# Performance work log

Hardware: AMD Instinct MI355X
Metric: run time of the kernel (lower is better)

## Reference

```python
import jax, jax.numpy as jnp
import numpy as np

B, H, L = 1024, 32, 3
D_S, D_ID = 512, 128
D_STEER = 3 * D_S + D_ID  # 1664
D_HID = 2048
HS, DQ = 16, 64
HDQ = HS * DQ  # 1024


def setup_inputs() -> dict:
    key = jax.random.key(0)
    ks = jax.random.split(key, 18)
    n = lambda k, shape, std: jax.random.normal(k, shape, dtype=jnp.float32) * std
    inp = {
        "x": jax.random.normal(ks[0], (B * H, D_STEER), dtype=jnp.float32),
        "id_in": jax.random.normal(ks[1], (B * H, D_ID), dtype=jnp.float32),
        # per-head content MLP params
        "in_proj_w": n(ks[2], (H, D_STEER, D_S), 0.014),
        "in_proj_b": jnp.zeros((H, D_S), jnp.float32),
        "norm_w": jnp.ones((H, L, D_S), jnp.float32),
        "up_w": n(ks[3], (H, L, D_S, D_HID), 0.014),
        "up_b": jnp.zeros((H, L, D_HID), jnp.float32),
        "down_w": n(ks[4], (H, L, D_HID, D_S), (2.0 / D_HID) ** 0.5),
        "down_b": jnp.zeros((H, L, D_S), jnp.float32),
        # q_proj: Linear(D_steer, 2*HDQ) -> GELU -> Linear(2*HDQ, HDQ)
        "q1_w": n(ks[5], (D_STEER, 2 * HDQ), 0.014),
        "q1_b": jnp.zeros((2 * HDQ,), jnp.float32),
        "q2_w": n(ks[6], (2 * HDQ, HDQ), 0.02),
        "q2_b": jnp.zeros((HDQ,), jnp.float32),
        # k_proj: Linear(D_id, 2*HDQ) -> GELU -> Linear(2*HDQ, HDQ)
        "k1_w": n(ks[7], (D_ID, 2 * HDQ), 0.014),
        "k1_b": jnp.zeros((2 * HDQ,), jnp.float32),
        "k2_w": n(ks[8], (2 * HDQ, HDQ), 0.02),
        "k2_b": jnp.zeros((HDQ,), jnp.float32),
    }
    return inp


def _per_head_mlp(x, in_proj_w, in_proj_b, norm_w, up_w, up_b, down_w, down_b):
    # x: [B*H, D_steer] -> [B*H, D_s]
    bh = x.shape[0]
    b = bh // H
    xh = x.reshape(b, H, D_STEER)
    h = jnp.einsum("bhd,hde->bhe", xh, in_proj_w) + in_proj_b[None]
    for i in range(norm_w.shape[1]):
        rms = jax.lax.rsqrt(jnp.mean(h * h, axis=-1, keepdims=True) + 1e-6)
        xn = h * rms * norm_w[:, i][None]
        hid = jax.nn.gelu(jnp.einsum("bhd,hde->bhe", xn, up_w[:, i]) + up_b[:, i][None], approximate=False)
        h = h + jnp.einsum("bhd,hde->bhe", hid, down_w[:, i]) + down_b[:, i][None]
    return h.reshape(bh, D_S)


def reference(x, id_in, in_proj_w, in_proj_b, norm_w, up_w, up_b, down_w, down_b,
              q1_w, q1_b, q2_w, q2_b, k1_w, k1_b, k2_w, k2_b):
    content = _per_head_mlp(x, in_proj_w, in_proj_b, norm_w, up_w, up_b, down_w, down_b)
    q = jax.nn.gelu(x @ q1_w + q1_b, approximate=False) @ q2_w + q2_b
    k = jax.nn.gelu(id_in @ k1_w + k1_b, approximate=False) @ k2_w + k2_b
    # concat outputs: [B*H, D_s + HDQ + HDQ]
    return jnp.concatenate([content, q, k], axis=-1)
```

## Files before the change

kernel.cpp:

```cpp
#include <hip/hip_runtime.h>
#include <hip/hip_bf16.h>
#include <math.h>

#define HH 32
#define LL 3
#define DS 512
#define DID 128
#define DSTEER 1664
#define DHID 2048
#define HDQ 1024
#define BHROWS 32768

typedef __attribute__((ext_vector_type(8))) short short8;
typedef __attribute__((ext_vector_type(4))) float f32x4;

typedef const __attribute__((address_space(1))) unsigned int* gptr_t;
typedef __attribute__((address_space(3))) unsigned int* lptr_t;

#define BAR() __builtin_amdgcn_s_barrier()
#define SB()  __builtin_amdgcn_sched_barrier(0)
#define VMCNT8() asm volatile("s_waitcnt vmcnt(8)")
#define VMCNT2() asm volatile("s_waitcnt vmcnt(2)")
#define VMCNT0() asm volatile("s_waitcnt vmcnt(0)")

__device__ __forceinline__ unsigned short f2bf(float f) {
  union { float f; unsigned int u; } x; x.f = f;
  unsigned int r = (x.u + 0x7FFFu + ((x.u >> 16) & 1u)) >> 16;
  return (unsigned short)r;
}
__device__ __forceinline__ unsigned int pk2(float a, float b) {
  return (unsigned int)f2bf(a) | ((unsigned int)f2bf(b) << 16);
}
__device__ __forceinline__ float gelu_exact(float v) {
  return 0.5f * v * (1.0f + erff(v * 0.70710678118654752440f));
}

__global__ void cvt_bf16_kernel(const float4* __restrict__ in, uint2* __restrict__ out, long n4) {
  long i = (long)blockIdx.x * blockDim.x + threadIdx.x;
  long stride = (long)gridDim.x * blockDim.x;
  for (; i < n4; i += stride) {
    float4 v = in[i];
    uint2 o; o.x = pk2(v.x, v.y); o.y = pk2(v.z, v.w);
    out[i] = o;
  }
}

__global__ void transpose_cvt_kernel(const float* __restrict__ in, long long in_bstride,
                                     unsigned short* __restrict__ out, long long out_bstride,
                                     int R, int C) {
  __shared__ float t[64][33];
  const int r0 = blockIdx.y * 32;
  const int c0 = blockIdx.x * 64;
  const float* bin = in + (long long)blockIdx.z * in_bstride;
  unsigned short* bout = out + (long long)blockIdx.z * out_bstride;
  const int tid = threadIdx.x;
  const int col = tid & 63, rr = tid >> 6;
  #pragma unroll
  for (int j = 0; j < 8; j++) {
    int r = j * 4 + rr;
    t[col][r] = bin[(size_t)(r0 + r) * C + c0 + col];
  }
  __syncthreads();
  const int rq = (tid & 7) * 4;
  const int cc = tid >> 3;
  #pragma unroll
  for (int j = 0; j < 2; j++) {
    int c = j * 32 + cc;
    float v0 = t[c][rq], v1 = t[c][rq + 1], v2 = t[c][rq + 2], v3 = t[c][rq + 3];
    uint2 o; o.x = pk2(v0, v1); o.y = pk2(v2, v3);
    *(uint2*)&bout[(size_t)(c0 + c) * R + r0 + rq] = o;
  }
}

__global__ void rms_scale_kernel(const float* __restrict__ h,
                                 const float* __restrict__ norm_w,
                                 unsigned short* __restrict__ xn, int layer) {
  int gw = (int)((blockIdx.x * blockDim.x + threadIdx.x) >> 6);
  int lane = threadIdx.x & 63;
  if (gw >= BHROWS) return;
  int head = gw & (HH - 1);
  const float4* hr = (const float4*)(h + (size_t)gw * DS);
  float4 v0 = hr[lane * 2], v1 = hr[lane * 2 + 1];
  float ss = v0.x*v0.x + v0.y*v0.y + v0.z*v0.z + v0.w*v0.w
           + v1.x*v1.x + v1.y*v1.y + v1.z*v1.z + v1.w*v1.w;
  #pragma unroll
  for (int off = 32; off > 0; off >>= 1) ss += __shfl_xor(ss, off, 64);
  float r = rsqrtf(ss * (1.0f / DS) + 1e-6f);
  const float4* nw = (const float4*)(norm_w + ((size_t)head * LL + layer) * DS);
  float4 w0 = nw[lane * 2], w1 = nw[lane * 2 + 1];
  uint4 o;
  o.x = pk2(v0.x * r * w0.x, v0.y * r * w0.y);
  o.y = pk2(v0.z * r * w0.z, v0.w * r * w0.w);
  o.z = pk2(v1.x * r * w1.x, v1.y * r * w1.y);
  o.w = pk2(v1.z * r * w1.z, v1.w * r * w1.w);
  *(uint4*)(xn + (size_t)gw * DS + (size_t)lane * 8) = o;
}

template<int EPI>
__global__ __launch_bounds__(512, 2)
void gemm256_kernel(const unsigned short* __restrict__ A, int lda, int rstep,
                    const unsigned short* __restrict__ Bt, int ldb, long long b_hstride,
                    const float* __restrict__ bias, int bias_hstride,
                    const float* __restrict__ resid, int ldr,
                    void* __restrict__ Cv, int ldc, int K) {
  __shared__ unsigned short lds[2 * 2 * 256 * 64];
  const int tid = threadIdx.x;
  const int lane = tid & 63;
  const int wave = tid >> 6;
  const int wr = wave >> 2, wc = wave & 3;
  const int head = blockIdx.z;
  const int gx = gridDim.x;
  const int nwg = gx * gridDim.y;
  int wgid = blockIdx.y * gx + blockIdx.x;
  { int cpx = nwg >> 3; wgid = (wgid & 7) * cpx + (wgid >> 3); }
  const int tn = wgid % gx, tm = wgid / gx;

  const int l3 = lane >> 3;
  const int gslot = ((lane & 7) ^ l3) * 8;
  const int mbase = wave * 8 + l3;
  const int nbase = (wave >> 2) * 64 + (wave & 3) * 8 + l3;
  const unsigned short* pA = A + ((size_t)(tm * 256 + mbase) * rstep + head) * lda + gslot;
  const unsigned short* pB = Bt + (size_t)head * b_hstride
                               + (size_t)(tn * 256 + nbase) * ldb + gslot;
  const size_t aBlk = (size_t)64 * rstep * lda;

  const int physk0 = ((lane >> 4) ^ (lane & 7)) * 8;
  const int physk1 = ((4 + (lane >> 4)) ^ (lane & 7)) * 8;
  const int aRow = wr * 128 + (lane & 15);
  const int bRow = wc * 32 + (lane & 15);

  auto stageA = [&](unsigned short* dstA, int h, size_t kels) {
    #pragma unroll
    for (int i = 0; i < 2; ++i)
      __builtin_amdgcn_global_load_lds(
          (gptr_t)(pA + (size_t)(i * 2 + h) * aBlk + kels),
          (lptr_t)(dstA + ((i * 2 + h) * 64 + wave * 8) * 64), 16, 0, 0);
  };
  auto stageB = [&](unsigned short* dstB, int h, size_t kels) {
    #pragma unroll
    for (int i = 0; i < 2; ++i)
      __builtin_amdgcn_global_load_lds(
          (gptr_t)(pB + (size_t)(i * 128 + h * 32) * ldb + kels),
          (lptr_t)(dstB + (h * 128 + i * 64 + wave * 8) * 64), 16, 0, 0);
  };

  f32x4 acc[8][4];
  #pragma unroll
  for (int i = 0; i < 8; ++i)
    #pragma unroll
    for (int j = 0; j < 4; ++j) acc[i][j] = (f32x4){0.f, 0.f, 0.f, 0.f};
  short8 a[4][2], b[4][2];

  const int T = K >> 6;
  stageA(lds, 0, 0);
  stageB(lds + 16384, 0, 0);
  stageB(lds + 16384, 1, 0);
  stageA(lds, 1, 0);
  stageA(lds + 32768, 0, 64);
  stageB(lds + 32768 + 16384, 0, 64);
  stageB(lds + 32768 + 16384, 1, 64);
  VMCNT8();
  SB();
  BAR();

  for (int t = 0; t < T; ++t) {
    unsigned short* rA = lds + (t & 1) * 32768;
    unsigned short* rB = rA + 16384;
    unsigned short* nA = lds + ((t + 1) & 1) * 32768;
    const size_t k1 = (size_t)(t + 1) * 64;
    const size_t k2 = (size_t)(t + 2) * 64;
    const bool m1 = (t + 1 < T), m2 = (t + 2 < T);

    #pragma unroll
    for (int j = 0; j < 2; ++j) {
      b[j][0] = *(const short8*)&rB[(bRow + j * 16) * 64 + physk0];
      b[j][1] = *(const short8*)&rB[(bRow + j * 16) * 64 + physk1];
    }
    #pragma unroll
    for (int i = 0; i < 4; ++i) {
      a[i][0] = *(const short8*)&rA[(aRow + i * 16) * 64 + physk0];
      a[i][1] = *(const short8*)&rA[(aRow + i * 16) * 64 + physk1];
    }
    if (m1) stageA(nA, 1, k1);
    __builtin_amdgcn_s_setprio(1);
    #pragma unroll
    for (int i = 0; i < 4; ++i)
      #pragma unroll
      for (int j = 0; j < 2; ++j) {
        acc[i][j] = __builtin_amdgcn_mfma_f32_16x16x32_bf16(a[i][0], b[j][0], acc[i][j], 0, 0, 0);
        acc[i][j] = __builtin_amdgcn_mfma_f32_16x16x32_bf16(a[i][1], b[j][1], acc[i][j], 0, 0, 0);
      }
    __builtin_amdgcn_s_setprio(0);
    BAR();

    #pragma unroll
    for (int j = 0; j < 2; ++j) {
      b[2 + j][0] = *(const short8*)&rB[(128 + bRow + j * 16) * 64 + physk0];
      b[2 + j][1] = *(const short8*)&rB[(128 + bRow + j * 16) * 64 + physk1];
    }
    __builtin_amdgcn_s_setprio(1);
    #pragma unroll
    for (int i = 0; i < 4; ++i)
      #pragma unroll
      for (int j = 0; j < 2; ++j) {
        acc[i][2 + j] = __builtin_amdgcn_mfma_f32_16x16x32_bf16(a[i][0], b[2 + j][0], acc[i][2 + j], 0, 0, 0);
        acc[i][2 + j] = __builtin_amdgcn_mfma_f32_16x16x32_bf16(a[i][1], b[2 + j][1], acc[i][2 + j], 0, 0, 0);
      }
    __builtin_amdgcn_s_setprio(0);
    if (m1) { VMCNT8(); } else { VMCNT0(); }
    SB();
    BAR();

    #pragma unroll
    for (int i = 0; i < 4; ++i) {
      a[i][0] = *(const short8*)&rA[(aRow + (4 + i) * 16) * 64 + physk0];
      a[i][1] = *(const short8*)&rA[(aRow + (4 + i) * 16) * 64 + physk1];
    }
    if (m2) { stageA(rA, 0, k2); stageB(rB, 0, k2); }
    __builtin_amdgcn_s_setprio(1);
    #pragma unroll
    for (int i = 0; i < 4; ++i)
      #pragma unroll
      for (int j = 0; j < 2; ++j) {
        acc[4 + i][2 + j] = __builtin_amdgcn_mfma_f32_16x16x32_bf16(a[i][0], b[2 + j][0], acc[4 + i][2 + j], 0, 0, 0);
        acc[4 + i][2 + j] = __builtin_amdgcn_mfma_f32_16x16x32_bf16(a[i][1], b[2 + j][1], acc[4 + i][2 + j], 0, 0, 0);
      }
    __builtin_amdgcn_s_setprio(0);
    BAR();

    if (m2) stageB(rB, 1, k2);
    __builtin_amdgcn_s_setprio(1);
    #pragma unroll
    for (int i = 0; i < 4; ++i)
      #pragma unroll
      for (int j = 0; j < 2; ++j) {
        acc[4 + i][j] = __builtin_amdgcn_mfma_f32_16x16x32_bf16(a[i][0], b[j][0], acc[4 + i][j], 0, 0, 0);
        acc[4 + i][j] = __builtin_amdgcn_mfma_f32_16x16x32_bf16(a[i][1], b[j][1], acc[4 + i][j], 0, 0, 0);
      }
    __builtin_amdgcn_s_setprio(0);
    if (m2) { VMCNT8(); } else if (m1) { VMCNT2(); }
    SB();
    BAR();
  }

  const float* bptr = bias + (size_t)head * bias_hstride;
  #pragma unroll
  for (int i = 0; i < 8; ++i) {
    #pragma unroll
    for (int j = 0; j < 4; ++j) {
      #pragma unroll
      for (int r = 0; r < 4; ++r) {
        int rowt = wr * 128 + i * 16 + (lane >> 4) * 4 + r;
        int colt = wc * 64 + j * 16 + (lane & 15);
        int col = tn * 256 + colt;
        size_t crow = (size_t)(tm * 256 + rowt) * rstep + head;
        float v = acc[i][j][r] + bptr[col];
        if (EPI == 1) {
          ((unsigned short*)Cv)[crow * (size_t)ldc + col] = f2bf(gelu_exact(v));
        } else if (EPI == 2) {
          v += resid[crow * (size_t)ldr + col];
          ((float*)Cv)[crow * (size_t)ldc + col] = v;
        } else {
          ((float*)Cv)[crow * (size_t)ldc + col] = v;
        }
      }
    }
  }
}

extern "C" void kernel_launch(void* const* d_in, const int* in_sizes, int n_in,
                              void* d_out, int out_size, void* d_ws, size_t ws_size,
                              hipStream_t stream) {
  const float* x         = (const float*)d_in[0];
  const float* id_in     = (const float*)d_in[1];
  const float* in_proj_w = (const float*)d_in[2];
  const float* in_proj_b = (const float*)d_in[3];
  const float* norm_w    = (const float*)d_in[4];
  const float* up_w      = (const float*)d_in[5];
  const float* up_b      = (const float*)d_in[6];
  const float* down_w    = (const float*)d_in[7];
  const float* down_b    = (const float*)d_in[8];
  const float* q1_w      = (const float*)d_in[9];
  const float* q1_b      = (const float*)d_in[10];
  const float* q2_w      = (const float*)d_in[11];
  const float* q2_b      = (const float*)d_in[12];
  const float* k1_w      = (const float*)d_in[13];
  const float* k1_b      = (const float*)d_in[14];
  const float* k2_w      = (const float*)d_in[15];
  const float* k2_b      = (const float*)d_in[16];
  float* out = (float*)d_out;

  char* ws = (char*)d_ws;
  unsigned short* x_bf  = (unsigned short*)ws; ws += (size_t)BHROWS * DSTEER * 2;
  unsigned short* id_bf = (unsigned short*)ws; ws += (size_t)BHROWS * DID * 2;
  float*          hbuf  = (float*)ws;          ws += (size_t)BHROWS * DS * 4;
  unsigned short* xn    = (unsigned short*)ws; ws += (size_t)BHROWS * DS * 2;
  unsigned short* hid   = (unsigned short*)ws; ws += (size_t)BHROWS * DHID * 2;
  unsigned short* wbuf  = (unsigned short*)ws; ws += (size_t)HH * DHID * DS * 2;

  cvt_bf16_kernel<<<2048, 256, 0, stream>>>((const float4*)x, (uint2*)x_bf,
                                            (long)BHROWS * DSTEER / 4);
  cvt_bf16_kernel<<<512, 256, 0, stream>>>((const float4*)id_in, (uint2*)id_bf,
                                           (long)BHROWS * DID / 4);

  transpose_cvt_kernel<<<dim3(2 * HDQ / 64, DSTEER / 32, 1), 256, 0, stream>>>(
      q1_w, 0, wbuf, 0, DSTEER, 2 * HDQ);
  gemm256_kernel<1><<<dim3(8, 128, 1), 512, 0, stream>>>(
      x_bf, DSTEER, 1, wbuf, DSTEER, 0, q1_b, 0, nullptr, 0, hid, 2 * HDQ, DSTEER);
  transpose_cvt_kernel<<<dim3(HDQ / 64, 2 * HDQ / 32, 1), 256, 0, stream>>>(
      q2_w, 0, wbuf, 0, 2 * HDQ, HDQ);
  gemm256_kernel<0><<<dim3(4, 128, 1), 512, 0, stream>>>(
      hid, 2 * HDQ, 1, wbuf, 2 * HDQ, 0, q2_b, 0, nullptr, 0, out + 512, 2560, 2 * HDQ);

  transpose_cvt_kernel<<<dim3(2 * HDQ / 64, DID / 32, 1), 256, 0, stream>>>(
      k1_w, 0, wbuf, 0, DID, 2 * HDQ);
  gemm256_kernel<1><<<dim3(8, 128, 1), 512, 0, stream>>>(
      id_bf, DID, 1, wbuf, DID, 0, k1_b, 0, nullptr, 0, hid, 2 * HDQ, DID);
  transpose_cvt_kernel<<<dim3(HDQ / 64, 2 * HDQ / 32, 1), 256, 0, stream>>>(
      k2_w, 0, wbuf, 0, 2 * HDQ, HDQ);
  gemm256_kernel<0><<<dim3(4, 128, 1), 512, 0, stream>>>(
      hid, 2 * HDQ, 1, wbuf, 2 * HDQ, 0, k2_b, 0, nullptr, 0, out + 1536, 2560, 2 * HDQ);

  transpose_cvt_kernel<<<dim3(DS / 64, DSTEER / 32, HH), 256, 0, stream>>>(
      in_proj_w, (long long)DSTEER * DS, wbuf, (long long)DS * DSTEER, DSTEER, DS);
  gemm256_kernel<0><<<dim3(2, 4, 32), 512, 0, stream>>>(
      x_bf, DSTEER, HH, wbuf, DSTEER, (long long)DS * DSTEER, in_proj_b, DS,
      nullptr, 0, hbuf, DS, DSTEER);

  for (int i = 0; i < LL; i++) {
    rms_scale_kernel<<<8192, 256, 0, stream>>>(hbuf, norm_w, xn, i);
    transpose_cvt_kernel<<<dim3(DHID / 64, DS / 32, HH), 256, 0, stream>>>(
        up_w + (size_t)i * DS * DHID, (long long)LL * DS * DHID,
        wbuf, (long long)DHID * DS, DS, DHID);
    gemm256_kernel<1><<<dim3(8, 4, 32), 512, 0, stream>>>(
        xn, DS, HH, wbuf, DS, (long long)DHID * DS,
        up_b + (size_t)i * DHID, LL * DHID, nullptr, 0, hid, DHID, DS);
    transpose_cvt_kernel<<<dim3(DS / 64, DHID / 32, HH), 256, 0, stream>>>(
        down_w + (size_t)i * DHID * DS, (long long)LL * DHID * DS,
        wbuf, (long long)DS * DHID, DHID, DS);
    float* cout = (i < 2) ? hbuf : out;
    int ldc = (i < 2) ? DS : 2560;
    gemm256_kernel<2><<<dim3(2, 4, 32), 512, 0, stream>>>(
        hid, DHID, HH, wbuf, DHID, (long long)DS * DHID,
        down_b + (size_t)i * DS, LL * DS, hbuf, DS, cout, ldc, DHID);
  }
}
```

Before: 1.694 ms.

## Switch GEMM to 32x32x16 MFMA and co-launch q1 with in_proj GEMM

Replaces the 16x16x32 MFMA tiling with 32x32x16 bf16 MFMA fragments. This cuts the number of LDS fragment reads and MFMA issues per tile. The GEMM kernel now takes a runtime job descriptor, so the q1 projection and the per-head in_proj GEMM run in a single launch, and the q2/k1/k2 weights are staged into the spare xn buffer. The costs are a runtime epilogue branch in place of the template, integer div/mod to map tiles, and more accumulator registers per fragment.

```diff
diff --git a/kernel.cpp b/kernel.cpp
--- a/kernel.cpp
+++ b/kernel.cpp
@@ -12,7 +12,7 @@
 #define BHROWS 32768
 
 typedef __attribute__((ext_vector_type(8))) short short8;
-typedef __attribute__((ext_vector_type(4))) float f32x4;
+typedef __attribute__((ext_vector_type(16))) float f32x16;
 
 typedef const __attribute__((address_space(1))) unsigned int* gptr_t;
 typedef __attribute__((address_space(3))) unsigned int* lptr_t;
@@ -96,38 +96,41 @@
   *(uint4*)(xn + (size_t)gw * DS + (size_t)lane * 8) = o;
 }
 
-template<int EPI>
+struct GJob {
+  const unsigned short* A; int lda; int rstep;
+  const unsigned short* Bt; long long b_hstride;
+  const float* bias; int bias_hstride;
+  const float* resid; int ldr;
+  void* C; int ldc;
+  int epi;
+  int gx;
+  int tph;
+};
+
 __global__ __launch_bounds__(512, 2)
-void gemm256_kernel(const unsigned short* __restrict__ A, int lda, int rstep,
-                    const unsigned short* __restrict__ Bt, int ldb, long long b_hstride,
-                    const float* __restrict__ bias, int bias_hstride,
-                    const float* __restrict__ resid, int ldr,
-                    void* __restrict__ Cv, int ldc, int K) {
+void gemm256_kernel(GJob j0, int n0, GJob j1, int K) {
   __shared__ unsigned short lds[2 * 2 * 256 * 64];
   const int tid = threadIdx.x;
   const int lane = tid & 63;
   const int wave = tid >> 6;
   const int wr = wave >> 2, wc = wave & 3;
-  const int head = blockIdx.z;
-  const int gx = gridDim.x;
-  const int nwg = gx * gridDim.y;
-  int wgid = blockIdx.y * gx + blockIdx.x;
-  { int cpx = nwg >> 3; wgid = (wgid & 7) * cpx + (wgid >> 3); }
-  const int tn = wgid % gx, tm = wgid / gx;
+  const int ntot = gridDim.x;
+  int wgid = blockIdx.x;
+  { int cpx = ntot >> 3; wgid = (wgid & 7) * cpx + (wgid >> 3); }
+  const GJob J = (wgid < n0) ? j0 : j1;
+  const int id = (wgid < n0) ? wgid : wgid - n0;
+  const int head = id / J.tph;
+  const int rem = id % J.tph;
+  const int tn = rem % J.gx, tm = rem / J.gx;
 
   const int l3 = lane >> 3;
   const int gslot = ((lane & 7) ^ l3) * 8;
   const int mbase = wave * 8 + l3;
   const int nbase = (wave >> 2) * 64 + (wave & 3) * 8 + l3;
-  const unsigned short* pA = A + ((size_t)(tm * 256 + mbase) * rstep + head) * lda + gslot;
-  const unsigned short* pB = Bt + (size_t)head * b_hstride
-                               + (size_t)(tn * 256 + nbase) * ldb + gslot;
-  const size_t aBlk = (size_t)64 * rstep * lda;
-
-  const int physk0 = ((lane >> 4) ^ (lane & 7)) * 8;
-  const int physk1 = ((4 + (lane >> 4)) ^ (lane & 7)) * 8;
-  const int aRow = wr * 128 + (lane & 15);
-  const int bRow = wc * 32 + (lane & 15);
+  const unsigned short* pA = J.A + ((size_t)(tm * 256 + mbase) * J.rstep + head) * J.lda + gslot;
+  const unsigned short* pB = J.Bt + (size_t)head * J.b_hstride
+                               + (size_t)(tn * 256 + nbase) * K + gslot;
+  const size_t aBlk = (size_t)64 * J.rstep * J.lda;
 
   auto stageA = [&](unsigned short* dstA, int h, size_t kels) {
     #pragma unroll
@@ -140,16 +143,25 @@
     #pragma unroll
     for (int i = 0; i < 2; ++i)
       __builtin_amdgcn_global_load_lds(
-          (gptr_t)(pB + (size_t)(i * 128 + h * 32) * ldb + kels),
+          (gptr_t)(pB + (size_t)(i * 128 + h * 32) * K + kels),
           (lptr_t)(dstB + (h * 128 + i * 64 + wave * 8) * 64), 16, 0, 0);
   };
 
-  f32x4 acc[8][4];
-  #pragma unroll
-  for (int i = 0; i < 8; ++i)
-    #pragma unroll
-    for (int j = 0; j < 4; ++j) acc[i][j] = (f32x4){0.f, 0.f, 0.f, 0.f};
-  short8 a[4][2], b[4][2];
+  const int aRowB = wr * 128 + (lane & 31);
+  const int bRowB = (wc >> 1) * 64 + (wc & 1) * 32 + (lane & 31);
+  const int kg = lane >> 5;
+  int physk[4];
+  #pragma unroll
+  for (int ks = 0; ks < 4; ++ks) physk[ks] = (((ks * 2 + kg) ^ (lane & 7)) * 8);
+
+  f32x16 acc[4][2];
+  #pragma unroll
+  for (int i = 0; i < 4; ++i)
+    #pragma unroll
+    for (int j = 0; j < 2; ++j)
+      #pragma unroll
+      for (int r = 0; r < 16; ++r) acc[i][j][r] = 0.f;
+  short8 aF[2][4], bL[4], bH[4];
 
   const int T = K >> 6;
   stageA(lds, 0, 0);
@@ -172,100 +184,98 @@
     const bool m1 = (t + 1 < T), m2 = (t + 2 < T);
 
     #pragma unroll
-    for (int j = 0; j < 2; ++j) {
-      b[j][0] = *(const short8*)&rB[(bRow + j * 16) * 64 + physk0];
-      b[j][1] = *(const short8*)&rB[(bRow + j * 16) * 64 + physk1];
-    }
-    #pragma unroll
-    for (int i = 0; i < 4; ++i) {
-      a[i][0] = *(const short8*)&rA[(aRow + i * 16) * 64 + physk0];
-      a[i][1] = *(const short8*)&rA[(aRow + i * 16) * 64 + physk1];
+    for (int ks = 0; ks < 4; ++ks) {
+      bL[ks] = *(const short8*)&rB[bRowB * 64 + physk[ks]];
+      aF[0][ks] = *(const short8*)&rA[aRowB * 64 + physk[ks]];
+      aF[1][ks] = *(const short8*)&rA[(aRowB + 32) * 64 + physk[ks]];
     }
     if (m1) stageA(nA, 1, k1);
     __builtin_amdgcn_s_setprio(1);
     #pragma unroll
-    for (int i = 0; i < 4; ++i)
-      #pragma unroll
-      for (int j = 0; j < 2; ++j) {
-        acc[i][j] = __builtin_amdgcn_mfma_f32_16x16x32_bf16(a[i][0], b[j][0], acc[i][j], 0, 0, 0);
-        acc[i][j] = __builtin_amdgcn_mfma_f32_16x16x32_bf16(a[i][1], b[j][1], acc[i][j], 0, 0, 0);
-      }
+    for (int mb = 0; mb < 2; ++mb)
+      #pragma unroll
+      for (int ks = 0; ks < 4; ++ks)
+        acc[mb][0] = __builtin_amdgcn_mfma_f32_32x32x16_bf16(aF[mb][ks], bL[ks], acc[mb][0], 0, 0, 0);
     __builtin_amdgcn_s_setprio(0);
     BAR();
 
     #pragma unroll
-    for (int j = 0; j < 2; ++j) {
-      b[2 + j][0] = *(const short8*)&rB[(128 + bRow + j * 16) * 64 + physk0];
-      b[2 + j][1] = *(const short8*)&rB[(128 + bRow + j * 16) * 64 + physk1];
-    }
+    for (int ks = 0; ks < 4; ++ks)
+      bH[ks] = *(const short8*)&rB[(128 + bRowB) * 64 + physk[ks]];
     __builtin_amdgcn_s_setprio(1);
     #pragma unroll
-    for (int i = 0; i < 4; ++i)
-      #pragma unroll
-      for (int j = 0; j < 2; ++j) {
-        acc[i][2 + j] = __builtin_amdgcn_mfma_f32_16x16x32_bf16(a[i][0], b[2 + j][0], acc[i][2 + j], 0, 0, 0);
-        acc[i][2 + j] = __builtin_amdgcn_mfma_f32_16x16x32_bf16(a[i][1], b[2 + j][1], acc[i][2 + j], 0, 0, 0);
-      }
+    for (int mb = 0; mb < 2; ++mb)
+      #pragma unroll
+      for (int ks = 0; ks < 4; ++ks)
+        acc[mb][1] = __builtin_amdgcn_mfma_f32_32x32x16_bf16(aF[mb][ks], bH[ks], acc[mb][1], 0, 0, 0);
     __builtin_amdgcn_s_setprio(0);
     if (m1) { VMCNT8(); } else { VMCNT0(); }
     SB();
     BAR();
 
     #pragma unroll
-    for (int i = 0; i < 4; ++i) {
-      a[i][0] = *(const short8*)&rA[(aRow + (4 + i) * 16) * 64 + physk0];
-      a[i][1] = *(const short8*)&rA[(aRow + (4 + i) * 16) * 64 + physk1];
+    for (int ks = 0; ks < 4; ++ks) {
+      aF[0][ks] = *(const short8*)&rA[(aRowB + 64) * 64 + physk[ks]];
+      aF[1][ks] = *(const short8*)&rA[(aRowB + 96) * 64 + physk[ks]];
     }
     if (m2) { stageA(rA, 0, k2); stageB(rB, 0, k2); }
     __builtin_amdgcn_s_setprio(1);
     #pragma unroll
-    for (int i = 0; i < 4; ++i)
-      #pragma unroll
-      for (int j = 0; j < 2; ++j) {
-        acc[4 + i][2 + j] = __builtin_amdgcn_mfma_f32_16x16x32_bf16(a[i][0], b[2 + j][0], acc[4 + i][2 + j], 0, 0, 0);
-        acc[4 + i][2 + j] = __builtin_amdgcn_mfma_f32_16x16x32_bf16(a[i][1], b[2 + j][1], acc[4 + i][2 + j], 0, 0, 0);
-      }
+    for (int mb = 0; mb < 2; ++mb)
+      #pragma unroll
+      for (int ks = 0; ks < 4; ++ks)
+        acc[2 + mb][1] = __builtin_amdgcn_mfma_f32_32x32x16_bf16(aF[mb][ks], bH[ks], acc[2 + mb][1], 0, 0, 0);
     __builtin_amdgcn_s_setprio(0);
     BAR();
 
     if (m2) stageB(rB, 1, k2);
     __builtin_amdgcn_s_setprio(1);
     #pragma unroll
-    for (int i = 0; i < 4; ++i)
-      #pragma unroll
-      for (int j = 0; j < 2; ++j) {
-        acc[4 + i][j] = __builtin_amdgcn_mfma_f32_16x16x32_bf16(a[i][0], b[j][0], acc[4 + i][j], 0, 0, 0);
-        acc[4 + i][j] = __builtin_amdgcn_mfma_f32_16x16x32_bf16(a[i][1], b[j][1], acc[4 + i][j], 0, 0, 0);
-      }
+    for (int mb = 0; mb < 2; ++mb)
+      #pragma unroll
+      for (int ks = 0; ks < 4; ++ks)
+        acc[2 + mb][0] = __builtin_amdgcn_mfma_f32_32x32x16_bf16(aF[mb][ks], bL[ks], acc[2 + mb][0], 0, 0, 0);
     __builtin_amdgcn_s_setprio(0);
     if (m2) { VMCNT8(); } else if (m1) { VMCNT2(); }
     SB();
     BAR();
   }
 
-  const float* bptr = bias + (size_t)head * bias_hstride;
-  #pragma unroll
-  for (int i = 0; i < 8; ++i) {
-    #pragma unroll
-    for (int j = 0; j < 4; ++j) {
-      #pragma unroll
-      for (int r = 0; r < 4; ++r) {
-        int rowt = wr * 128 + i * 16 + (lane >> 4) * 4 + r;
-        int colt = wc * 64 + j * 16 + (lane & 15);
-        int col = tn * 256 + colt;
-        size_t crow = (size_t)(tm * 256 + rowt) * rstep + head;
+  const float* bptr = J.bias + (size_t)head * J.bias_hstride;
+  const int rbase = wr * 128 + 4 * (lane >> 5);
+  const int cbase = tn * 256 + wc * 64 + (lane & 31);
+  #pragma unroll
+  for (int i = 0; i < 4; ++i) {
+    #pragma unroll
+    for (int j = 0; j < 2; ++j) {
+      #pragma unroll
+      for (int r = 0; r < 16; ++r) {
+        int rowt = rbase + i * 32 + (r & 3) + 8 * (r >> 2);
+        int col = cbase + j * 32;
+        size_t crow = (size_t)(tm * 256 + rowt) * J.rstep + head;
         float v = acc[i][j][r] + bptr[col];
-        if (EPI == 1) {
-          ((unsigned short*)Cv)[crow * (size_t)ldc + col] = f2bf(gelu_exact(v));
-        } else if (EPI == 2) {
-          v += resid[crow * (size_t)ldr + col];
-          ((float*)Cv)[crow * (size_t)ldc + col] = v;
+        if (J.epi == 1) {
+          ((unsigned short*)J.C)[crow * (size_t)J.ldc + col] = f2bf(gelu_exact(v));
+        } else if (J.epi == 2) {
+          v += J.resid[crow * (size_t)J.ldr + col];
+          ((float*)J.C)[crow * (size_t)J.ldc + col] = v;
         } else {
-          ((float*)Cv)[crow * (size_t)ldc + col] = v;
+          ((float*)J.C)[crow * (size_t)J.ldc + col] = v;
         }
       }
     }
   }
+}
+
+static inline GJob mkjob(const unsigned short* A, int lda, int rstep,
+                         const unsigned short* Bt, long long hstride,
+                         const float* bias, int bias_h,
+                         const float* resid, int ldr,
+                         void* C, int ldc, int epi, int gx, int gy) {
+  GJob j; j.A = A; j.lda = lda; j.rstep = rstep; j.Bt = Bt; j.b_hstride = hstride;
+  j.bias = bias; j.bias_hstride = bias_h; j.resid = resid; j.ldr = ldr;
+  j.C = C; j.ldc = ldc; j.epi = epi; j.gx = gx; j.tph = gx * gy;
+  return j;
 }
 
 extern "C" void kernel_launch(void* const* d_in, const int* in_sizes, int n_in,
@@ -298,50 +308,72 @@
   unsigned short* hid   = (unsigned short*)ws; ws += (size_t)BHROWS * DHID * 2;
   unsigned short* wbuf  = (unsigned short*)ws; ws += (size_t)HH * DHID * DS * 2;
 
+  unsigned short* q1w_t  = wbuf;
+  unsigned short* ipw_t  = wbuf + (size_t)DSTEER * 2 * HDQ;
+  unsigned short* q2w_t  = xn;
+  unsigned short* k1w_t  = xn + (size_t)2 * HDQ * HDQ;
+  unsigned short* k2w_t  = xn + (size_t)2 * HDQ * HDQ + (size_t)2 * HDQ * DID;
+
   cvt_bf16_kernel<<<2048, 256, 0, stream>>>((const float4*)x, (uint2*)x_bf,
                                             (long)BHROWS * DSTEER / 4);
   cvt_bf16_kernel<<<512, 256, 0, stream>>>((const float4*)id_in, (uint2*)id_bf,
                                            (long)BHROWS * DID / 4);
 
   transpose_cvt_kernel<<<dim3(2 * HDQ / 64, DSTEER / 32, 1), 256, 0, stream>>>(
-      q1_w, 0, wbuf, 0, DSTEER, 2 * HDQ);
-  gemm256_kernel<1><<<dim3(8, 128, 1), 512, 0, stream>>>(
-      x_bf, DSTEER, 1, wbuf, DSTEER, 0, q1_b, 0, nullptr, 0, hid, 2 * HDQ, DSTEER);
+      q1_w, 0, q1w_t, 0, DSTEER, 2 * HDQ);
+  transpose_cvt_kernel<<<dim3(DS / 64, DSTEER / 32, HH), 256, 0, stream>>>(
+      in_proj_w, (long long)DSTEER * DS, ipw_t, (long long)DS * DSTEER, DSTEER, DS);
   transpose_cvt_kernel<<<dim3(HDQ / 64, 2 * HDQ / 32, 1), 256, 0, stream>>>(
-      q2_w, 0, wbuf, 0, 2 * HDQ, HDQ);
-  gemm256_kernel<0><<<dim3(4, 128, 1), 512, 0, stream>>>(
-      hid, 2 * HDQ, 1, wbuf, 2 * HDQ, 0, q2_b, 0, nullptr, 0, out + 512, 2560, 2 * HDQ);
-
+      q2_w, 0, q2w_t, 0, 2 * HDQ, HDQ);
   transpose_cvt_kernel<<<dim3(2 * HDQ / 64, DID / 32, 1), 256, 0, stream>>>(
-      k1_w, 0, wbuf, 0, DID, 2 * HDQ);
-  gemm256_kernel<1><<<dim3(8, 128, 1), 512, 0, stream>>>(
-      id_bf, DID, 1, wbuf, DID, 0, k1_b, 0, nullptr, 0, hid, 2 * HDQ, DID);
+      k1_w, 0, k1w_t, 0, DID, 2 * HDQ);
   transpose_cvt_kernel<<<dim3(HDQ / 64, 2 * HDQ / 32, 1), 256, 0, stream>>>(
-      k2_w, 0, wbuf, 0, 2 * HDQ, HDQ);
-  gemm256_kernel<0><<<dim3(4, 128, 1), 512, 0, stream>>>(
-      hid, 2 * HDQ, 1, wbuf, 2 * HDQ, 0, k2_b, 0, nullptr, 0, out + 1536, 2560, 2 * HDQ);
-
-  transpose_cvt_kernel<<<dim3(DS / 64, DSTEER / 32, HH), 256, 0, stream>>>(
-      in_proj_w, (long long)DSTEER * DS, wbuf, (long long)DS * DSTEER, DSTEER, DS);
-  gemm256_kernel<0><<<dim3(2, 4, 32), 512, 0, stream>>>(
-      x_bf, DSTEER, HH, wbuf, DSTEER, (long long)DS * DSTEER, in_proj_b, DS,
-      nullptr, 0, hbuf, DS, DSTEER);
+      k2_w, 0, k2w_t, 0, 2 * HDQ, HDQ);
+
+  {
+    GJob jq1 = mkjob(x_bf, DSTEER, 1, q1w_t, 0, q1_b, 0, nullptr, 0,
+                     hid, 2 * HDQ, 1, 8, 128);
+    GJob jip = mkjob(x_bf, DSTEER, HH, ipw_t, (long long)DS * DSTEER, in_proj_b, DS,
+                     nullptr, 0, hbuf, DS, 0, 2, 4);
+    gemm256_kernel<<<1280, 512, 0, stream>>>(jq1, 1024, jip, DSTEER);
+  }
+  {
+    GJob j = mkjob(hid, 2 * HDQ, 1, q2w_t, 0, q2_b, 0, nullptr, 0,
+                   out + 512, 2560, 0, 4, 128);
+    gemm256_kernel<<<512, 512, 0, stream>>>(j, 512, j, 2 * HDQ);
+  }
+  {
+    GJob j = mkjob(id_bf, DID, 1, k1w_t, 0, k1_b, 0, nullptr, 0,
+                   hid, 2 * HDQ, 1, 8, 128);
+    gemm256_kernel<<<1024, 512, 0, stream>>>(j, 1024, j, DID);
+  }
+  {
+    GJob j = mkjob(hid, 2 * HDQ, 1, k2w_t, 0, k2_b, 0, nullptr, 0,
+                   out + 1536, 2560, 0, 4, 128);
+    gemm256_kernel<<<512, 512, 0, stream>>>(j, 512, j, 2 * HDQ);
+  }
 
   for (int i = 0; i < LL; i++) {
     rms_scale_kernel<<<8192, 256, 0, stream>>>(hbuf, norm_w, xn, i);
     transpose_cvt_kernel<<<dim3(DHID / 64, DS / 32, HH), 256, 0, stream>>>(
         up_w + (size_t)i * DS * DHID, (long long)LL * DS * DHID,
         wbuf, (long long)DHID * DS, DS, DHID);
-    gemm256_kernel<1><<<dim3(8, 4, 32), 512, 0, stream>>>(
-        xn, DS, HH, wbuf, DS, (long long)DHID * DS,
-        up_b + (size_t)i * DHID, LL * DHID, nullptr, 0, hid, DHID, DS);
+    {
+      GJob j = mkjob(xn, DS, HH, wbuf, (long long)DHID * DS,
+                     up_b + (size_t)i * DHID, LL * DHID, nullptr, 0,
+                     hid, DHID, 1, 8, 4);
+      gemm256_kernel<<<1024, 512, 0, stream>>>(j, 1024, j, DS);
+    }
     transpose_cvt_kernel<<<dim3(DS / 64, DHID / 32, HH), 256, 0, stream>>>(
         down_w + (size_t)i * DHID * DS, (long long)LL * DHID * DS,
         wbuf, (long long)DS * DHID, DHID, DS);
-    float* cout = (i < 2) ? hbuf : out;
-    int ldc = (i < 2) ? DS : 2560;
-    gemm256_kernel<2><<<dim3(2, 4, 32), 512, 0, stream>>>(
-        hid, DHID, HH, wbuf, DHID, (long long)DS * DHID,
-        down_b + (size_t)i * DS, LL * DS, hbuf, DS, cout, ldc, DHID);
-  }
-}
+    {
+      float* cout = (i < 2) ? hbuf : out;
+      int ldc = (i < 2) ? DS : 2560;
+      GJob j = mkjob(hid, DHID, HH, wbuf, (long long)DS * DHID,
+                     down_b + (size_t)i * DS, LL * DS, hbuf, DS,
+                     cout, ldc, 2, 2, 4);
+      gemm256_kernel<<<256, 512, 0, stream>>>(j, 256, j, DHID);
+    }
+  }
+}
```

Result: slower. 2.488 ms (+46.9%).

## Batch independent GEMMs into shared grouped launches with runtime job dispatch

Applied to the files above, without the earlier changes.

Turns the GEMM kernel into a grouped kernel that takes two job descriptors and sends each workgroup to one of them. Independent GEMMs (q1 with in_proj, q2 with k1, k2 with the first up-projection) now run in a single launch. This fills the GPU better and removes launch gaps, especially for the small per-head GEMMs with 256 workgroups. To make the pairs possible, transposed weights are staged into reused workspace regions, and an extra hidden buffer is used when the workspace is large enough. The epilogue type is now a runtime value instead of a template parameter, which adds branches and may cost registers.

```diff
diff --git a/kernel.cpp b/kernel.cpp
--- a/kernel.cpp
+++ b/kernel.cpp
@@ -96,33 +96,43 @@
   *(uint4*)(xn + (size_t)gw * DS + (size_t)lane * 8) = o;
 }
 
-template<int EPI>
+struct GJob {
+  const unsigned short* A; int lda; int rstep;
+  const unsigned short* Bt; long long b_hstride;
+  const float* bias; int bias_hstride;
+  const float* resid; int ldr;
+  void* C; int ldc;
+  int epi;
+  int gx;
+  int tph;
+  int K;
+};
+
 __global__ __launch_bounds__(512, 2)
-void gemm256_kernel(const unsigned short* __restrict__ A, int lda, int rstep,
-                    const unsigned short* __restrict__ Bt, int ldb, long long b_hstride,
-                    const float* __restrict__ bias, int bias_hstride,
-                    const float* __restrict__ resid, int ldr,
-                    void* __restrict__ Cv, int ldc, int K) {
+void gemm256_kernel(GJob j0, int n0, GJob j1) {
   __shared__ unsigned short lds[2 * 2 * 256 * 64];
   const int tid = threadIdx.x;
   const int lane = tid & 63;
   const int wave = tid >> 6;
   const int wr = wave >> 2, wc = wave & 3;
-  const int head = blockIdx.z;
-  const int gx = gridDim.x;
-  const int nwg = gx * gridDim.y;
-  int wgid = blockIdx.y * gx + blockIdx.x;
-  { int cpx = nwg >> 3; wgid = (wgid & 7) * cpx + (wgid >> 3); }
-  const int tn = wgid % gx, tm = wgid / gx;
+  const int ntot = gridDim.x;
+  int wgid = blockIdx.x;
+  { int cpx = ntot >> 3; wgid = (wgid & 7) * cpx + (wgid >> 3); }
+  const GJob J = (wgid < n0) ? j0 : j1;
+  const int id = (wgid < n0) ? wgid : wgid - n0;
+  const int head = id / J.tph;
+  const int rem = id % J.tph;
+  const int tn = rem % J.gx, tm = rem / J.gx;
+  const int K = J.K;
 
   const int l3 = lane >> 3;
   const int gslot = ((lane & 7) ^ l3) * 8;
   const int mbase = wave * 8 + l3;
   const int nbase = (wave >> 2) * 64 + (wave & 3) * 8 + l3;
-  const unsigned short* pA = A + ((size_t)(tm * 256 + mbase) * rstep + head) * lda + gslot;
-  const unsigned short* pB = Bt + (size_t)head * b_hstride
-                               + (size_t)(tn * 256 + nbase) * ldb + gslot;
-  const size_t aBlk = (size_t)64 * rstep * lda;
+  const unsigned short* pA = J.A + ((size_t)(tm * 256 + mbase) * J.rstep + head) * J.lda + gslot;
+  const unsigned short* pB = J.Bt + (size_t)head * J.b_hstride
+                               + (size_t)(tn * 256 + nbase) * K + gslot;
+  const size_t aBlk = (size_t)64 * J.rstep * J.lda;
 
   const int physk0 = ((lane >> 4) ^ (lane & 7)) * 8;
   const int physk1 = ((4 + (lane >> 4)) ^ (lane & 7)) * 8;
@@ -140,7 +150,7 @@
     #pragma unroll
     for (int i = 0; i < 2; ++i)
       __builtin_amdgcn_global_load_lds(
-          (gptr_t)(pB + (size_t)(i * 128 + h * 32) * ldb + kels),
+          (gptr_t)(pB + (size_t)(i * 128 + h * 32) * K + kels),
           (lptr_t)(dstB + (h * 128 + i * 64 + wave * 8) * 64), 16, 0, 0);
   };
 
@@ -243,7 +253,7 @@
     BAR();
   }
 
-  const float* bptr = bias + (size_t)head * bias_hstride;
+  const float* bptr = J.bias + (size_t)head * J.bias_hstride;
   #pragma unroll
   for (int i = 0; i < 8; ++i) {
     #pragma unroll
@@ -253,19 +263,30 @@
         int rowt = wr * 128 + i * 16 + (lane >> 4) * 4 + r;
         int colt = wc * 64 + j * 16 + (lane & 15);
         int col = tn * 256 + colt;
-        size_t crow = (size_t)(tm * 256 + rowt) * rstep + head;
+        size_t crow = (size_t)(tm * 256 + rowt) * J.rstep + head;
         float v = acc[i][j][r] + bptr[col];
-        if (EPI == 1) {
-          ((unsigned short*)Cv)[crow * (size_t)ldc + col] = f2bf(gelu_exact(v));
-        } else if (EPI == 2) {
-          v += resid[crow * (size_t)ldr + col];
-          ((float*)Cv)[crow * (size_t)ldc + col] = v;
+        if (J.epi == 1) {
+          ((unsigned short*)J.C)[crow * (size_t)J.ldc + col] = f2bf(gelu_exact(v));
+        } else if (J.epi == 2) {
+          v += J.resid[crow * (size_t)J.ldr + col];
+          ((float*)J.C)[crow * (size_t)J.ldc + col] = v;
         } else {
-          ((float*)Cv)[crow * (size_t)ldc + col] = v;
+          ((float*)J.C)[crow * (size_t)J.ldc + col] = v;
         }
       }
     }
   }
+}
+
+static inline GJob mkjob(const unsigned short* A, int lda, int rstep,
+                         const unsigned short* Bt, long long hstride,
+                         const float* bias, int bias_h,
+                         const float* resid, int ldr,
+                         void* C, int ldc, int epi, int gx, int tph, int K) {
+  GJob j; j.A = A; j.lda = lda; j.rstep = rstep; j.Bt = Bt; j.b_hstride = hstride;
+  j.bias = bias; j.bias_hstride = bias_h; j.resid = resid; j.ldr = ldr;
+  j.C = C; j.ldc = ldc; j.epi = epi; j.gx = gx; j.tph = tph; j.K = K;
+  return j;
 }
 
 extern "C" void kernel_launch(void* const* d_in, const int* in_sizes, int n_in,
@@ -297,6 +318,15 @@
   unsigned short* xn    = (unsigned short*)ws; ws += (size_t)BHROWS * DS * 2;
   unsigned short* hid   = (unsigned short*)ws; ws += (size_t)BHROWS * DHID * 2;
   unsigned short* wbuf  = (unsigned short*)ws; ws += (size_t)HH * DHID * DS * 2;
+  size_t base_bytes = (size_t)(ws - (char*)d_ws);
+  bool big = ws_size >= base_bytes + (size_t)BHROWS * DHID * 2;
+  unsigned short* hid_k = big ? (unsigned short*)ws : hid;
+
+  unsigned short* q1w_t = wbuf;
+  unsigned short* ipw_t = wbuf + (size_t)DSTEER * 2 * HDQ;
+  unsigned short* q2w_t = xn;
+  unsigned short* k1w_t = xn + (size_t)2 * HDQ * HDQ;
+  unsigned short* k2w_t = id_bf;
 
   cvt_bf16_kernel<<<2048, 256, 0, stream>>>((const float4*)x, (uint2*)x_bf,
                                             (long)BHROWS * DSTEER / 4);
@@ -304,44 +334,73 @@
                                            (long)BHROWS * DID / 4);
 
   transpose_cvt_kernel<<<dim3(2 * HDQ / 64, DSTEER / 32, 1), 256, 0, stream>>>(
-      q1_w, 0, wbuf, 0, DSTEER, 2 * HDQ);
-  gemm256_kernel<1><<<dim3(8, 128, 1), 512, 0, stream>>>(
-      x_bf, DSTEER, 1, wbuf, DSTEER, 0, q1_b, 0, nullptr, 0, hid, 2 * HDQ, DSTEER);
+      q1_w, 0, q1w_t, 0, DSTEER, 2 * HDQ);
+  transpose_cvt_kernel<<<dim3(DS / 64, DSTEER / 32, HH), 256, 0, stream>>>(
+      in_proj_w, (long long)DSTEER * DS, ipw_t, (long long)DS * DSTEER, DSTEER, DS);
+
+  {
+    GJob jq1 = mkjob(x_bf, DSTEER, 1, q1w_t, 0, q1_b, 0, nullptr, 0,
+                     hid, 2 * HDQ, 1, 8, 1024, DSTEER);
+    GJob jip = mkjob(x_bf, DSTEER, HH, ipw_t, (long long)DS * DSTEER, in_proj_b, DS,
+                     nullptr, 0, hbuf, DS, 0, 2, 8, DSTEER);
+    gemm256_kernel<<<1280, 512, 0, stream>>>(jq1, 1024, jip);
+  }
+
   transpose_cvt_kernel<<<dim3(HDQ / 64, 2 * HDQ / 32, 1), 256, 0, stream>>>(
-      q2_w, 0, wbuf, 0, 2 * HDQ, HDQ);
-  gemm256_kernel<0><<<dim3(4, 128, 1), 512, 0, stream>>>(
-      hid, 2 * HDQ, 1, wbuf, 2 * HDQ, 0, q2_b, 0, nullptr, 0, out + 512, 2560, 2 * HDQ);
-
+      q2_w, 0, q2w_t, 0, 2 * HDQ, HDQ);
   transpose_cvt_kernel<<<dim3(2 * HDQ / 64, DID / 32, 1), 256, 0, stream>>>(
-      k1_w, 0, wbuf, 0, DID, 2 * HDQ);
-  gemm256_kernel<1><<<dim3(8, 128, 1), 512, 0, stream>>>(
-      id_bf, DID, 1, wbuf, DID, 0, k1_b, 0, nullptr, 0, hid, 2 * HDQ, DID);
-  transpose_cvt_kernel<<<dim3(HDQ / 64, 2 * HDQ / 32, 1), 256, 0, stream>>>(
-      k2_w, 0, wbuf, 0, 2 * HDQ, HDQ);
-  gemm256_kernel<0><<<dim3(4, 128, 1), 512, 0, stream>>>(
-      hid, 2 * HDQ, 1, wbuf, 2 * HDQ, 0, k2_b, 0, nullptr, 0, out + 1536, 2560, 2 * HDQ);
-
-  transpose_cvt_kernel<<<dim3(DS / 64, DSTEER / 32, HH), 256, 0, stream>>>(
-      in_proj_w, (long long)DSTEER * DS, wbuf, (long long)DS * DSTEER, DSTEER, DS);
-  gemm256_kernel<0><<<dim3(2, 4, 32), 512, 0, stream>>>(
-      x_bf, DSTEER, HH, wbuf, DSTEER, (long long)DS * DSTEER, in_proj_b, DS,
-      nullptr, 0, hbuf, DS, DSTEER);
+      k1_w, 0, k1w_t, 0, DID, 2 * HDQ);
+
+  GJob jq2 = mkjob(hid, 2 * HDQ, 1, q2w_t, 0, q2_b, 0, nullptr, 0,
+                   out + 512, 2560, 0, 4, 512, 2 * HDQ);
+  GJob jk1 = mkjob(id_bf, DID, 1, k1w_t, 0, k1_b, 0, nullptr, 0,
+                   hid_k, 2 * HDQ, 1, 8, 1024, DID);
+  GJob jk2 = mkjob(hid_k, 2 * HDQ, 1, k2w_t, 0, k2_b, 0, nullptr, 0,
+                   out + 1536, 2560, 0, 4, 512, 2 * HDQ);
+
+  if (big) {
+    gemm256_kernel<<<1536, 512, 0, stream>>>(jq2, 512, jk1);
+    rms_scale_kernel<<<8192, 256, 0, stream>>>(hbuf, norm_w, xn, 0);
+    transpose_cvt_kernel<<<dim3(DHID / 64, DS / 32, HH), 256, 0, stream>>>(
+        up_w, (long long)LL * DS * DHID, wbuf, (long long)DHID * DS, DS, DHID);
+    transpose_cvt_kernel<<<dim3(HDQ / 64, 2 * HDQ / 32, 1), 256, 0, stream>>>(
+        k2_w, 0, k2w_t, 0, 2 * HDQ, HDQ);
+    GJob jup0 = mkjob(xn, DS, HH, wbuf, (long long)DHID * DS, up_b, LL * DHID,
+                      nullptr, 0, hid, DHID, 1, 8, 32, DS);
+    gemm256_kernel<<<1536, 512, 0, stream>>>(jk2, 512, jup0);
+  } else {
+    gemm256_kernel<<<512, 512, 0, stream>>>(jq2, 512, jq2);
+    gemm256_kernel<<<1024, 512, 0, stream>>>(jk1, 1024, jk1);
+    transpose_cvt_kernel<<<dim3(HDQ / 64, 2 * HDQ / 32, 1), 256, 0, stream>>>(
+        k2_w, 0, k2w_t, 0, 2 * HDQ, HDQ);
+    gemm256_kernel<<<512, 512, 0, stream>>>(jk2, 512, jk2);
+    rms_scale_kernel<<<8192, 256, 0, stream>>>(hbuf, norm_w, xn, 0);
+    transpose_cvt_kernel<<<dim3(DHID / 64, DS / 32, HH), 256, 0, stream>>>(
+        up_w, (long long)LL * DS * DHID, wbuf, (long long)DHID * DS, DS, DHID);
+    GJob jup0 = mkjob(xn, DS, HH, wbuf, (long long)DHID * DS, up_b, LL * DHID,
+                      nullptr, 0, hid, DHID, 1, 8, 32, DS);
+    gemm256_kernel<<<1024, 512, 0, stream>>>(jup0, 1024, jup0);
+  }
 
   for (int i = 0; i < LL; i++) {
-    rms_scale_kernel<<<8192, 256, 0, stream>>>(hbuf, norm_w, xn, i);
-    transpose_cvt_kernel<<<dim3(DHID / 64, DS / 32, HH), 256, 0, stream>>>(
-        up_w + (size_t)i * DS * DHID, (long long)LL * DS * DHID,
-        wbuf, (long long)DHID * DS, DS, DHID);
-    gemm256_kernel<1><<<dim3(8, 4, 32), 512, 0, stream>>>(
-        xn, DS, HH, wbuf, DS, (long long)DHID * DS,
-        up_b + (size_t)i * DHID, LL * DHID, nullptr, 0, hid, DHID, DS);
+    if (i > 0) {
+      rms_scale_kernel<<<8192, 256, 0, stream>>>(hbuf, norm_w, xn, i);
+      transpose_cvt_kernel<<<dim3(DHID / 64, DS / 32, HH), 256, 0, stream>>>(
+          up_w + (size_t)i * DS * DHID, (long long)LL * DS * DHID,
+          wbuf, (long long)DHID * DS, DS, DHID);
+      GJob jup = mkjob(xn, DS, HH, wbuf, (long long)DHID * DS,
+                       up_b + (size_t)i * DHID, LL * DHID, nullptr, 0,
+                       hid, DHID, 1, 8, 32, DS);
+      gemm256_kernel<<<1024, 512, 0, stream>>>(jup, 1024, jup);
+    }
     transpose_cvt_kernel<<<dim3(DS / 64, DHID / 32, HH), 256, 0, stream>>>(
         down_w + (size_t)i * DHID * DS, (long long)LL * DHID * DS,
         wbuf, (long long)DS * DHID, DHID, DS);
     float* cout = (i < 2) ? hbuf : out;
     int ldc = (i < 2) ? DS : 2560;
-    gemm256_kernel<2><<<dim3(2, 4, 32), 512, 0, stream>>>(
-        hid, DHID, HH, wbuf, DHID, (long long)DS * DHID,
-        down_b + (size_t)i * DS, LL * DS, hbuf, DS, cout, ldc, DHID);
-  }
-}
+    GJob jdn = mkjob(hid, DHID, HH, wbuf, (long long)DS * DHID,
+                     down_b + (size_t)i * DS, LL * DS, hbuf, DS,
+                     cout, ldc, 2, 2, 8, DHID);
+    gemm256_kernel<<<256, 512, 0, stream>>>(jdn, 256, jdn);
+  }
+}
```

Measured after the change: 2.581 ms. 1.52x slower.

## Store per-head intermediates head-major and flatten GEMM grid with XCD swizzle

Applied to the files above, without the earlier changes.

Intermediate activations (hbuf, xn, hid) for the per-head MLP are now laid out head-major, [head][batch][dim], instead of interleaved rows with stride 32. The A, residual and C operands therefore read and write contiguous rows rather than rows strided by H. The GEMM launches now use a flat 1-D grid, and the 8-way swizzle that spreads blocks across XCDs is applied over all heads together, not per head. The price is more general stride arithmetic, and the final layer's epilogue must scatter back into the interleaved output layout.

```diff
diff --git a/kernel.cpp b/kernel.cpp
--- a/kernel.cpp
+++ b/kernel.cpp
@@ -78,7 +78,7 @@
   int gw = (int)((blockIdx.x * blockDim.x + threadIdx.x) >> 6);
   int lane = threadIdx.x & 63;
   if (gw >= BHROWS) return;
-  int head = gw & (HH - 1);
+  int head = gw >> 10;
   const float4* hr = (const float4*)(h + (size_t)gw * DS);
   float4 v0 = hr[lane * 2], v1 = hr[lane * 2 + 1];
   float ss = v0.x*v0.x + v0.y*v0.y + v0.z*v0.z + v0.w*v0.w
@@ -98,31 +98,33 @@
 
 template<int EPI>
 __global__ __launch_bounds__(512, 2)
-void gemm256_kernel(const unsigned short* __restrict__ A, int lda, int rstep,
-                    const unsigned short* __restrict__ Bt, int ldb, long long b_hstride,
+void gemm256_kernel(const unsigned short* __restrict__ A, long long a_hstride, long long a_rstride,
+                    const unsigned short* __restrict__ Bt, long long b_hstride,
                     const float* __restrict__ bias, int bias_hstride,
-                    const float* __restrict__ resid, int ldr,
-                    void* __restrict__ Cv, int ldc, int K) {
+                    const float* __restrict__ resid, long long r_hstride, long long r_rstride,
+                    void* __restrict__ Cv, long long c_hstride, long long c_rstride,
+                    int gx, int tph, int K) {
   __shared__ unsigned short lds[2 * 2 * 256 * 64];
   const int tid = threadIdx.x;
   const int lane = tid & 63;
   const int wave = tid >> 6;
   const int wr = wave >> 2, wc = wave & 3;
-  const int head = blockIdx.z;
-  const int gx = gridDim.x;
-  const int nwg = gx * gridDim.y;
-  int wgid = blockIdx.y * gx + blockIdx.x;
-  { int cpx = nwg >> 3; wgid = (wgid & 7) * cpx + (wgid >> 3); }
-  const int tn = wgid % gx, tm = wgid / gx;
+  const int ntot = gridDim.x;
+  int id = blockIdx.x;
+  { int cpx = ntot >> 3; id = (id & 7) * cpx + (id >> 3); }
+  const int head = id / tph;
+  const int rem = id % tph;
+  const int tn = rem % gx, tm = rem / gx;
 
   const int l3 = lane >> 3;
   const int gslot = ((lane & 7) ^ l3) * 8;
   const int mbase = wave * 8 + l3;
   const int nbase = (wave >> 2) * 64 + (wave & 3) * 8 + l3;
-  const unsigned short* pA = A + ((size_t)(tm * 256 + mbase) * rstep + head) * lda + gslot;
+  const unsigned short* pA = A + (size_t)head * a_hstride
+                               + (size_t)(tm * 256 + mbase) * a_rstride + gslot;
   const unsigned short* pB = Bt + (size_t)head * b_hstride
-                               + (size_t)(tn * 256 + nbase) * ldb + gslot;
-  const size_t aBlk = (size_t)64 * rstep * lda;
+                               + (size_t)(tn * 256 + nbase) * K + gslot;
+  const size_t aBlk = (size_t)64 * a_rstride;
 
   const int physk0 = ((lane >> 4) ^ (lane & 7)) * 8;
   const int physk1 = ((4 + (lane >> 4)) ^ (lane & 7)) * 8;
@@ -140,7 +142,7 @@
     #pragma unroll
     for (int i = 0; i < 2; ++i)
       __builtin_amdgcn_global_load_lds(
-          (gptr_t)(pB + (size_t)(i * 128 + h * 32) * ldb + kels),
+          (gptr_t)(pB + (size_t)(i * 128 + h * 32) * K + kels),
           (lptr_t)(dstB + (h * 128 + i * 64 + wave * 8) * 64), 16, 0, 0);
   };
 
@@ -253,15 +255,16 @@
         int rowt = wr * 128 + i * 16 + (lane >> 4) * 4 + r;
         int colt = wc * 64 + j * 16 + (lane & 15);
         int col = tn * 256 + colt;
-        size_t crow = (size_t)(tm * 256 + rowt) * rstep + head;
+        size_t row = (size_t)(tm * 256 + rowt);
+        size_t cidx = (size_t)head * c_hstride + row * c_rstride + col;
         float v = acc[i][j][r] + bptr[col];
         if (EPI == 1) {
-          ((unsigned short*)Cv)[crow * (size_t)ldc + col] = f2bf(gelu_exact(v));
+          ((unsigned short*)Cv)[cidx] = f2bf(gelu_exact(v));
         } else if (EPI == 2) {
-          v += resid[crow * (size_t)ldr + col];
-          ((float*)Cv)[crow * (size_t)ldc + col] = v;
+          v += resid[(size_t)head * r_hstride + row * r_rstride + col];
+          ((float*)Cv)[cidx] = v;
         } else {
-          ((float*)Cv)[crow * (size_t)ldc + col] = v;
+          ((float*)Cv)[cidx] = v;
         }
       }
     }
@@ -305,43 +308,57 @@
 
   transpose_cvt_kernel<<<dim3(2 * HDQ / 64, DSTEER / 32, 1), 256, 0, stream>>>(
       q1_w, 0, wbuf, 0, DSTEER, 2 * HDQ);
-  gemm256_kernel<1><<<dim3(8, 128, 1), 512, 0, stream>>>(
-      x_bf, DSTEER, 1, wbuf, DSTEER, 0, q1_b, 0, nullptr, 0, hid, 2 * HDQ, DSTEER);
+  gemm256_kernel<1><<<1024, 512, 0, stream>>>(
+      x_bf, 0, DSTEER, wbuf, 0, q1_b, 0, nullptr, 0, 0,
+      hid, 0, 2 * HDQ, 8, 1024, DSTEER);
   transpose_cvt_kernel<<<dim3(HDQ / 64, 2 * HDQ / 32, 1), 256, 0, stream>>>(
       q2_w, 0, wbuf, 0, 2 * HDQ, HDQ);
-  gemm256_kernel<0><<<dim3(4, 128, 1), 512, 0, stream>>>(
-      hid, 2 * HDQ, 1, wbuf, 2 * HDQ, 0, q2_b, 0, nullptr, 0, out + 512, 2560, 2 * HDQ);
+  gemm256_kernel<0><<<512, 512, 0, stream>>>(
+      hid, 0, 2 * HDQ, wbuf, 0, q2_b, 0, nullptr, 0, 0,
+      out + 512, 0, 2560, 4, 512, 2 * HDQ);
 
   transpose_cvt_kernel<<<dim3(2 * HDQ / 64, DID / 32, 1), 256, 0, stream>>>(
       k1_w, 0, wbuf, 0, DID, 2 * HDQ);
-  gemm256_kernel<1><<<dim3(8, 128, 1), 512, 0, stream>>>(
-      id_bf, DID, 1, wbuf, DID, 0, k1_b, 0, nullptr, 0, hid, 2 * HDQ, DID);
+  gemm256_kernel<1><<<1024, 512, 0, stream>>>(
+      id_bf, 0, DID, wbuf, 0, k1_b, 0, nullptr, 0, 0,
+      hid, 0, 2 * HDQ, 8, 1024, DID);
   transpose_cvt_kernel<<<dim3(HDQ / 64, 2 * HDQ / 32, 1), 256, 0, stream>>>(
       k2_w, 0, wbuf, 0, 2 * HDQ, HDQ);
-  gemm256_kernel<0><<<dim3(4, 128, 1), 512, 0, stream>>>(
-      hid, 2 * HDQ, 1, wbuf, 2 * HDQ, 0, k2_b, 0, nullptr, 0, out + 1536, 2560, 2 * HDQ);
+  gemm256_kernel<0><<<512, 512, 0, stream>>>(
+      hid, 0, 2 * HDQ, wbuf, 0, k2_b, 0, nullptr, 0, 0,
+      out + 1536, 0, 2560, 4, 512, 2 * HDQ);
 
   transpose_cvt_kernel<<<dim3(DS / 64, DSTEER / 32, HH), 256, 0, stream>>>(
       in_proj_w, (long long)DSTEER * DS, wbuf, (long long)DS * DSTEER, DSTEER, DS);
-  gemm256_kernel<0><<<dim3(2, 4, 32), 512, 0, stream>>>(
-      x_bf, DSTEER, HH, wbuf, DSTEER, (long long)DS * DSTEER, in_proj_b, DS,
-      nullptr, 0, hbuf, DS, DSTEER);
+  gemm256_kernel<0><<<256, 512, 0, stream>>>(
+      x_bf, DSTEER, (long long)32 * DSTEER, wbuf, (long long)DS * DSTEER,
+      in_proj_b, DS, nullptr, 0, 0,
+      hbuf, (long long)1024 * DS, DS, 2, 8, DSTEER);
 
   for (int i = 0; i < LL; i++) {
     rms_scale_kernel<<<8192, 256, 0, stream>>>(hbuf, norm_w, xn, i);
     transpose_cvt_kernel<<<dim3(DHID / 64, DS / 32, HH), 256, 0, stream>>>(
         up_w + (size_t)i * DS * DHID, (long long)LL * DS * DHID,
         wbuf, (long long)DHID * DS, DS, DHID);
-    gemm256_kernel<1><<<dim3(8, 4, 32), 512, 0, stream>>>(
-        xn, DS, HH, wbuf, DS, (long long)DHID * DS,
-        up_b + (size_t)i * DHID, LL * DHID, nullptr, 0, hid, DHID, DS);
+    gemm256_kernel<1><<<1024, 512, 0, stream>>>(
+        xn, (long long)1024 * DS, DS, wbuf, (long long)DHID * DS,
+        up_b + (size_t)i * DHID, LL * DHID, nullptr, 0, 0,
+        hid, (long long)1024 * DHID, DHID, 8, 32, DS);
     transpose_cvt_kernel<<<dim3(DS / 64, DHID / 32, HH), 256, 0, stream>>>(
         down_w + (size_t)i * DHID * DS, (long long)LL * DHID * DS,
         wbuf, (long long)DS * DHID, DHID, DS);
-    float* cout = (i < 2) ? hbuf : out;
-    int ldc = (i < 2) ? DS : 2560;
-    gemm256_kernel<2><<<dim3(2, 4, 32), 512, 0, stream>>>(
-        hid, DHID, HH, wbuf, DHID, (long long)DS * DHID,
-        down_b + (size_t)i * DS, LL * DS, hbuf, DS, cout, ldc, DHID);
-  }
-}
+    if (i < 2) {
+      gemm256_kernel<2><<<256, 512, 0, stream>>>(
+          hid, (long long)1024 * DHID, DHID, wbuf, (long long)DS * DHID,
+          down_b + (size_t)i * DS, LL * DS,
+          hbuf, (long long)1024 * DS, DS,
+          hbuf, (long long)1024 * DS, DS, 2, 8, DHID);
+    } else {
+      gemm256_kernel<2><<<256, 512, 0, stream>>>(
+          hid, (long long)1024 * DHID, DHID, wbuf, (long long)DS * DHID,
+          down_b + (size_t)i * DS, LL * DS,
+          hbuf, (long long)1024 * DS, DS,
+          out, 2560, (long long)32 * 2560, 2, 8, DHID);
+    }
+  }
+}
```

Result: faster. 1.614 ms (-4.7%).
